# Performance work log

Hardware: AMD Instinct MI355X
Metric: run time of the kernel (lower is better)

Reference implementation:

```python
import jax, jax.numpy as jnp
import numpy as np

WINDOW_SIZE = 11
SIGMA = 1.5

def _gaussian_window(size, sigma):
    coords = jnp.arange(size, dtype=jnp.float32) - size // 2
    g = jnp.exp(-coords ** 2 / (2.0 * sigma ** 2))
    g = g / g.sum()
    return jnp.outer(g, g)  # [size, size]

def _depthwise_conv(x, win2d):
    # x: [B, C, H, W]; win2d: [K, K]; depthwise (groups=C), SAME padding
    C = x.shape[1]
    K = win2d.shape[0]
    kernel = jnp.broadcast_to(win2d[None, None], (C, 1, K, K))  # [C,1,K,K] (OIHW, I=1 per group)
    pad = K // 2
    return jax.lax.conv_general_dilated(
        x, kernel,
        window_strides=(1, 1),
        padding=((pad, pad), (pad, pad)),
        dimension_numbers=('NCHW', 'OIHW', 'NCHW'),
        feature_group_count=C)

def setup_inputs() -> dict:
    key = jax.random.key(0)
    k1, k2 = jax.random.split(key)
    pred = jax.random.uniform(k1, (8, 4, 512, 512), dtype=jnp.float32)
    target = jax.random.uniform(k2, (8, 4, 512, 512), dtype=jnp.float32)
    return {"pred": pred, "target": target}

def reference(pred, target):
    win = _gaussian_window(WINDOW_SIZE, SIGMA)
    mu1 = _depthwise_conv(pred, win)
    mu2 = _depthwise_conv(target, win)
    mu1_sq = mu1 * mu1
    mu2_sq = mu2 * mu2
    mu1_mu2 = mu1 * mu2
    sigma1_sq = _depthwise_conv(pred * pred, win) - mu1_sq
    sigma2_sq = _depthwise_conv(target * target, win) - mu2_sq
    sigma12 = _depthwise_conv(pred * target, win) - mu1_mu2
    C1 = 0.01 ** 2
    C2 = 0.03 ** 2
    ssim_map = ((2.0 * mu1_mu2 + C1) * (2.0 * sigma12 + C2)) / (
        (mu1_sq + mu2_sq + C1) * (sigma1_sq + sigma2_sq + C2))
    return 1.0 - ssim_map.mean()
```

## Files before the change

kernel.cpp:

```cpp
#include <hip/hip_runtime.h>
#include <cmath>

#define IMG_H 512
#define IMG_W 512
#define TILE_X 64
#define TILE_Y 32
#define LH 42
#define LW 74
#define LSTRIDE 76
#define NBLOCKS (8 * 16 * 32)
#define NPIX (8 * 4 * 512 * 512)

struct Weights { float w[11]; };

__global__ __launch_bounds__(256, 2)
void ssim_tile_kernel(const float* __restrict__ pred,
                      const float* __restrict__ targ,
                      float* __restrict__ partials,
                      Weights wt)
{
    __shared__ float sp[LH * LSTRIDE];
    __shared__ float st[LH * LSTRIDE];
    __shared__ float h1[LH * TILE_X];
    __shared__ float h2[LH * TILE_X];
    __shared__ float h11[LH * TILE_X];
    __shared__ float h22[LH * TILE_X];
    __shared__ float h12[LH * TILE_X];
    __shared__ float wsum[4];

    const int tid = threadIdx.x;
    const int x0 = blockIdx.x * TILE_X;
    const int y0 = blockIdx.y * TILE_Y;
    const int plane = blockIdx.z;
    const float* __restrict__ P = pred + (size_t)plane * IMG_H * IMG_W;
    const float* __restrict__ T = targ + (size_t)plane * IMG_H * IMG_W;

    for (int i = tid; i < LH * LW; i += 256) {
        int r = i / LW;
        int c = i - r * LW;
        int gy = y0 + r - 5;
        int gx = x0 + c - 5;
        float p = 0.f, t = 0.f;
        if (((unsigned)gy < IMG_H) & ((unsigned)gx < IMG_W)) {
            p = P[gy * IMG_W + gx];
            t = T[gy * IMG_W + gx];
        }
        sp[r * LSTRIDE + c] = p;
        st[r * LSTRIDE + c] = t;
    }
    __syncthreads();

    for (int i = tid; i < LH * 16; i += 256) {
        int r = i >> 4;
        int c4 = (i & 15) * 4;
        const float* rp = sp + r * LSTRIDE + c4;
        const float* rt = st + r * LSTRIDE + c4;
        float p[16], t[16];
        #pragma unroll
        for (int q = 0; q < 4; ++q) {
            *(float4*)&p[q * 4] = *(const float4*)&rp[q * 4];
            *(float4*)&t[q * 4] = *(const float4*)&rt[q * 4];
        }
        float s1[4], s2[4], s11[4], s22[4], s12[4];
        #pragma unroll
        for (int o = 0; o < 4; ++o) { s1[o]=0.f; s2[o]=0.f; s11[o]=0.f; s22[o]=0.f; s12[o]=0.f; }
        #pragma unroll
        for (int k = 0; k < 11; ++k) {
            float w = wt.w[k];
            #pragma unroll
            for (int o = 0; o < 4; ++o) {
                float pv = p[o + k], tv = t[o + k];
                float wp = w * pv, wtv = w * tv;
                s1[o]  += wp;
                s2[o]  += wtv;
                s11[o] += wp * pv;
                s22[o] += wtv * tv;
                s12[o] += wp * tv;
            }
        }
        int ho = r * TILE_X + c4;
        *(float4*)&h1[ho]  = make_float4(s1[0],  s1[1],  s1[2],  s1[3]);
        *(float4*)&h2[ho]  = make_float4(s2[0],  s2[1],  s2[2],  s2[3]);
        *(float4*)&h11[ho] = make_float4(s11[0], s11[1], s11[2], s11[3]);
        *(float4*)&h22[ho] = make_float4(s22[0], s22[1], s22[2], s22[3]);
        *(float4*)&h12[ho] = make_float4(s12[0], s12[1], s12[2], s12[3]);
    }
    __syncthreads();

    const int c  = tid & 63;
    const int r0 = (tid >> 6) * 8;
    float a1[8], a2[8], a11[8], a22[8], a12[8];
    #pragma unroll
    for (int o = 0; o < 8; ++o) { a1[o]=0.f; a2[o]=0.f; a11[o]=0.f; a22[o]=0.f; a12[o]=0.f; }

    #pragma unroll
    for (int j = 0; j < 18; ++j) {
        int hr = (r0 + j) * TILE_X + c;
        float v1  = h1[hr];
        float v2  = h2[hr];
        float v11 = h11[hr];
        float v22 = h22[hr];
        float v12 = h12[hr];
        #pragma unroll
        for (int o = 0; o < 8; ++o) {
            int k = j - o;
            if (k >= 0 && k < 11) {
                float w = wt.w[k];
                a1[o]  += w * v1;
                a2[o]  += w * v2;
                a11[o] += w * v11;
                a22[o] += w * v22;
                a12[o] += w * v12;
            }
        }
    }

    float lsum = 0.f;
    #pragma unroll
    for (int o = 0; o < 8; ++o) {
        float mu1 = a1[o], mu2 = a2[o];
        float m11 = mu1 * mu1, m22 = mu2 * mu2, m12 = mu1 * mu2;
        float sg1 = a11[o] - m11;
        float sg2 = a22[o] - m22;
        float sg12 = a12[o] - m12;
        float num = (2.f * m12 + 1e-4f) * (2.f * sg12 + 9e-4f);
        float den = (m11 + m22 + 1e-4f) * (sg1 + sg2 + 9e-4f);
        lsum += num / den;
    }

    #pragma unroll
    for (int off = 32; off > 0; off >>= 1) lsum += __shfl_down(lsum, off);
    if ((tid & 63) == 0) wsum[tid >> 6] = lsum;
    __syncthreads();
    if (tid == 0) {
        float bsum = wsum[0] + wsum[1] + wsum[2] + wsum[3];
        partials[(blockIdx.z * gridDim.y + blockIdx.y) * gridDim.x + blockIdx.x] = bsum;
    }
}

__global__ void ssim_finalize(const float* __restrict__ partials, float* __restrict__ out)
{
    __shared__ double red[256];
    double s = 0.0;
    for (int i = threadIdx.x; i < NBLOCKS; i += 256) s += (double)partials[i];
    red[threadIdx.x] = s;
    __syncthreads();
    for (int stride = 128; stride > 0; stride >>= 1) {
        if ((int)threadIdx.x < stride) red[threadIdx.x] += red[threadIdx.x + stride];
        __syncthreads();
    }
    if (threadIdx.x == 0) out[0] = (float)(1.0 - red[0] / (double)NPIX);
}

extern "C" void kernel_launch(void* const* d_in, const int* in_sizes, int n_in,
                              void* d_out, int out_size, void* d_ws, size_t ws_size,
                              hipStream_t stream) {
    const float* pred = (const float*)d_in[0];
    const float* targ = (const float*)d_in[1];
    float* out = (float*)d_out;
    float* partials = (float*)d_ws;

    Weights wt;
    {
        float g[11];
        float s = 0.f;
        for (int i = 0; i < 11; ++i) {
            float d = (float)(i - 5);
            g[i] = expf(-d * d / (2.f * 1.5f * 1.5f));
            s += g[i];
        }
        for (int i = 0; i < 11; ++i) wt.w[i] = g[i] / s;
    }

    dim3 grid(IMG_W / TILE_X, IMG_H / TILE_Y, 32);
    ssim_tile_kernel<<<grid, 256, 0, stream>>>(pred, targ, partials, wt);
    ssim_finalize<<<1, 256, 0, stream>>>(partials, out);
}
```

Before: 90.81 us.

## Load horizontal-pass inputs directly from global memory and double block size

Removes the shared-memory staging of the raw pred/target tiles. The horizontal pass now reads 20-wide aligned float4 windows straight from global memory, with a scalar fallback at image edges. Blocks grow to 512 threads, each handling 4 output rows instead of 8 in the vertical pass, to raise occupancy and cut per-thread register pressure. The trade-off is redundant global/L2 reads from overlapping windows and divergent edge paths in exchange for less LDS traffic and one fewer barrier.

```diff
diff --git a/kernel.cpp b/kernel.cpp
--- a/kernel.cpp
+++ b/kernel.cpp
@@ -6,27 +6,23 @@
 #define TILE_X 64
 #define TILE_Y 32
 #define LH 42
-#define LW 74
-#define LSTRIDE 76
 #define NBLOCKS (8 * 16 * 32)
 #define NPIX (8 * 4 * 512 * 512)
 
 struct Weights { float w[11]; };
 
-__global__ __launch_bounds__(256, 2)
+__global__ __launch_bounds__(512, 4)
 void ssim_tile_kernel(const float* __restrict__ pred,
                       const float* __restrict__ targ,
                       float* __restrict__ partials,
                       Weights wt)
 {
-    __shared__ float sp[LH * LSTRIDE];
-    __shared__ float st[LH * LSTRIDE];
     __shared__ float h1[LH * TILE_X];
     __shared__ float h2[LH * TILE_X];
     __shared__ float h11[LH * TILE_X];
     __shared__ float h22[LH * TILE_X];
     __shared__ float h12[LH * TILE_X];
-    __shared__ float wsum[4];
+    __shared__ float wsum[8];
 
     const int tid = threadIdx.x;
     const int x0 = blockIdx.x * TILE_X;
@@ -35,32 +31,35 @@
     const float* __restrict__ P = pred + (size_t)plane * IMG_H * IMG_W;
     const float* __restrict__ T = targ + (size_t)plane * IMG_H * IMG_W;
 
-    for (int i = tid; i < LH * LW; i += 256) {
-        int r = i / LW;
-        int c = i - r * LW;
-        int gy = y0 + r - 5;
-        int gx = x0 + c - 5;
-        float p = 0.f, t = 0.f;
-        if (((unsigned)gy < IMG_H) & ((unsigned)gx < IMG_W)) {
-            p = P[gy * IMG_W + gx];
-            t = T[gy * IMG_W + gx];
-        }
-        sp[r * LSTRIDE + c] = p;
-        st[r * LSTRIDE + c] = t;
-    }
-    __syncthreads();
-
-    for (int i = tid; i < LH * 16; i += 256) {
+    for (int i = tid; i < LH * 16; i += 512) {
         int r = i >> 4;
         int c4 = (i & 15) * 4;
-        const float* rp = sp + r * LSTRIDE + c4;
-        const float* rt = st + r * LSTRIDE + c4;
-        float p[16], t[16];
-        #pragma unroll
-        for (int q = 0; q < 4; ++q) {
-            *(float4*)&p[q * 4] = *(const float4*)&rp[q * 4];
-            *(float4*)&t[q * 4] = *(const float4*)&rt[q * 4];
+        int gy = y0 + r - 5;
+        float p[20], t[20];
+        if ((unsigned)gy < IMG_H) {
+            const float* rp = P + gy * IMG_W;
+            const float* rt = T + gy * IMG_W;
+            int gx0 = x0 + c4 - 8;
+            if (gx0 >= 0 && gx0 + 20 <= IMG_W) {
+                #pragma unroll
+                for (int q = 0; q < 5; ++q) {
+                    *(float4*)&p[q * 4] = *(const float4*)&rp[gx0 + q * 4];
+                    *(float4*)&t[q * 4] = *(const float4*)&rt[gx0 + q * 4];
+                }
+            } else {
+                #pragma unroll
+                for (int q = 0; q < 20; ++q) {
+                    int gx = gx0 + q;
+                    bool v = (unsigned)gx < IMG_W;
+                    p[q] = v ? rp[gx] : 0.f;
+                    t[q] = v ? rt[gx] : 0.f;
+                }
+            }
+        } else {
+            #pragma unroll
+            for (int q = 0; q < 20; ++q) { p[q] = 0.f; t[q] = 0.f; }
         }
+
         float s1[4], s2[4], s11[4], s22[4], s12[4];
         #pragma unroll
         for (int o = 0; o < 4; ++o) { s1[o]=0.f; s2[o]=0.f; s11[o]=0.f; s22[o]=0.f; s12[o]=0.f; }
@@ -69,7 +68,7 @@
             float w = wt.w[k];
             #pragma unroll
             for (int o = 0; o < 4; ++o) {
-                float pv = p[o + k], tv = t[o + k];
+                float pv = p[o + 3 + k], tv = t[o + 3 + k];
                 float wp = w * pv, wtv = w * tv;
                 s1[o]  += wp;
                 s2[o]  += wtv;
@@ -88,13 +87,13 @@
     __syncthreads();
 
     const int c  = tid & 63;
-    const int r0 = (tid >> 6) * 8;
-    float a1[8], a2[8], a11[8], a22[8], a12[8];
+    const int r0 = (tid >> 6) * 4;
+    float a1[4], a2[4], a11[4], a22[4], a12[4];
     #pragma unroll
-    for (int o = 0; o < 8; ++o) { a1[o]=0.f; a2[o]=0.f; a11[o]=0.f; a22[o]=0.f; a12[o]=0.f; }
+    for (int o = 0; o < 4; ++o) { a1[o]=0.f; a2[o]=0.f; a11[o]=0.f; a22[o]=0.f; a12[o]=0.f; }
 
     #pragma unroll
-    for (int j = 0; j < 18; ++j) {
+    for (int j = 0; j < 14; ++j) {
         int hr = (r0 + j) * TILE_X + c;
         float v1  = h1[hr];
         float v2  = h2[hr];
@@ -102,7 +101,7 @@
         float v22 = h22[hr];
         float v12 = h12[hr];
         #pragma unroll
-        for (int o = 0; o < 8; ++o) {
+        for (int o = 0; o < 4; ++o) {
             int k = j - o;
             if (k >= 0 && k < 11) {
                 float w = wt.w[k];
@@ -117,7 +116,7 @@
 
     float lsum = 0.f;
     #pragma unroll
-    for (int o = 0; o < 8; ++o) {
+    for (int o = 0; o < 4; ++o) {
         float mu1 = a1[o], mu2 = a2[o];
         float m11 = mu1 * mu1, m22 = mu2 * mu2, m12 = mu1 * mu2;
         float sg1 = a11[o] - m11;
@@ -133,7 +132,9 @@
     if ((tid & 63) == 0) wsum[tid >> 6] = lsum;
     __syncthreads();
     if (tid == 0) {
-        float bsum = wsum[0] + wsum[1] + wsum[2] + wsum[3];
+        float bsum = 0.f;
+        #pragma unroll
+        for (int wv = 0; wv < 8; ++wv) bsum += wsum[wv];
         partials[(blockIdx.z * gridDim.y + blockIdx.y) * gridDim.x + blockIdx.x] = bsum;
     }
 }
@@ -173,6 +174,6 @@
     }
 
     dim3 grid(IMG_W / TILE_X, IMG_H / TILE_Y, 32);
-    ssim_tile_kernel<<<grid, 256, 0, stream>>>(pred, targ, partials, wt);
+    ssim_tile_kernel<<<grid, 512, 0, stream>>>(pred, targ, partials, wt);
     ssim_finalize<<<1, 256, 0, stream>>>(partials, out);
 }
```

After: 73.13 us. 19.5% less time.
